# Kernel tuning notes

Hardware: AMD Instinct MI355X
Metric: run time of the kernel (lower is better)

## Reference

```python
import jax, jax.numpy as jnp
import numpy as np

B, N, C = 4, 2048, 1024
H = 16
D = C // H  # head_dim = 64
NEG = -1e9


def setup_inputs() -> dict:
    key = jax.random.key(0)
    k1, k2, k3, k4 = jax.random.split(key, 4)
    x = jax.random.normal(k1, (B, N, C), dtype=jnp.float32)
    # additive causal mask [N, N]: 0 on/below diagonal, -1e9 above
    causal = jnp.tril(jnp.ones((N, N), dtype=bool))
    attn_mask = jnp.where(causal, 0.0, NEG).astype(jnp.float32)
    # params: qkv Dense (no bias, qkv_bias=False), proj Dense (with bias)
    W_qkv = jax.random.normal(k2, (C, 3 * C), dtype=jnp.float32) / np.sqrt(C)
    W_proj = jax.random.normal(k3, (C, C), dtype=jnp.float32) / np.sqrt(C)
    b_proj = jnp.zeros((C,), dtype=jnp.float32)
    return {"x": x, "attn_mask": attn_mask, "W_qkv": W_qkv,
            "W_proj": W_proj, "b_proj": b_proj}


def reference(x, attn_mask, W_qkv, W_proj, b_proj):
    b, n, c = x.shape
    # qkv projection -> [B, N, 3, H, D] -> q,k,v each [B, H, N, D]
    qkv = (x @ W_qkv).reshape(b, n, 3, H, D)
    qkv = jnp.transpose(qkv, (2, 0, 3, 1, 4))
    q, k, v = qkv[0], qkv[1], qkv[2]
    # unfused attention: full [B, H, N, N] score matrix
    scores = jnp.einsum('bhnd,bhmd->bhnm', q, k) / np.sqrt(D).astype(jnp.float32)
    scores = scores + attn_mask  # broadcast [N, N] over batch/heads
    attn_w = jax.nn.softmax(scores.astype(jnp.float32), axis=-1).astype(scores.dtype)
    out = jnp.einsum('bhnm,bhmd->bhnd', attn_w, v)
    out = jnp.transpose(out, (0, 2, 1, 3)).reshape(b, n, c)
    return out @ W_proj + b_proj
```

## Files before the change

kernel.cpp:

```cpp
#include <hip/hip_runtime.h>
#include <stdint.h>


typedef short s16x8 __attribute__((ext_vector_type(8)));
typedef short s16x4 __attribute__((ext_vector_type(4)));
typedef float f32x4 __attribute__((ext_vector_type(4)));
typedef unsigned int u32;

__device__ __forceinline__ uint16_t f2bf(float f) {
  union { float f; uint32_t u; } v; v.f = f;
  uint32_t r = v.u + 0x7fffu + ((v.u >> 16) & 1u);
  return (uint16_t)(r >> 16);
}

__device__ __forceinline__ u32 cvt_pk_bf16(float lo, float hi) {
  u32 r;
  asm("v_cvt_pk_bf16_f32 %0, %1, %2" : "=v"(r) : "v"(lo), "v"(hi));
  return r;
}

__device__ __forceinline__ s16x8 pack4(u32 w0, u32 w1, u32 w2, u32 w3) {
  union { u32 u[4]; s16x8 v; } t;
  t.u[0] = w0; t.u[1] = w1; t.u[2] = w2; t.u[3] = w3;
  return t.v;
}

__device__ __forceinline__ s16x8 pack2h(s16x4 a, s16x4 b) {
  union { s16x4 h[2]; s16x8 v; } t;
  t.h[0] = a; t.h[1] = b;
  return t.v;
}

#define GLOAD_LDS16(g, l)                                            \
  __builtin_amdgcn_global_load_lds(                                  \
      (const __attribute__((address_space(1))) void*)(g),            \
      (__attribute__((address_space(3))) void*)(l), 16, 0, 0)

__device__ __forceinline__ void transpose32_body(
    const float* __restrict__ src, uint16_t* __restrict__ dst,
    int R, int C, int bx32, int by32, uint16_t (*tile)[33], int tid) {
  const int tx = tid & 31, ty = tid >> 5;
#pragma unroll
  for (int i = 0; i < 32; i += 8)
    tile[ty + i][tx] = f2bf(src[(size_t)(by32 + ty + i) * C + bx32 + tx]);
  __syncthreads();
#pragma unroll
  for (int i = 0; i < 32; i += 8)
    dst[(size_t)(bx32 + ty + i) * R + by32 + tx] = tile[tx][ty + i];
}

__global__ __launch_bounds__(256) void prep_kernel(
    const float* __restrict__ x, uint16_t* __restrict__ xbf,
    const float* __restrict__ Wqkv, uint16_t* __restrict__ wqkvT,
    const float* __restrict__ Wproj, uint16_t* __restrict__ wprojT) {
  __shared__ uint16_t tile[32][33];
  const int bid = blockIdx.x;
  if (bid < 4096) {
    const int i = bid * 256 + threadIdx.x;
    const f32x4 a = ((const f32x4*)x)[2 * i];
    const f32x4 b = ((const f32x4*)x)[2 * i + 1];
    s16x8 r;
    r[0] = (short)f2bf(a[0]); r[1] = (short)f2bf(a[1]);
    r[2] = (short)f2bf(a[2]); r[3] = (short)f2bf(a[3]);
    r[4] = (short)f2bf(b[0]); r[5] = (short)f2bf(b[1]);
    r[6] = (short)f2bf(b[2]); r[7] = (short)f2bf(b[3]);
    ((s16x8*)xbf)[i] = r;
  } else if (bid < 4096 + 3072) {
    const int t = bid - 4096;
    transpose32_body(Wqkv, wqkvT, 1024, 3072, (t % 96) * 32, (t / 96) * 32,
                     tile, threadIdx.x);
  } else {
    const int t = bid - 7168;
    transpose32_body(Wproj, wprojT, 1024, 1024, (t & 31) * 32, (t >> 5) * 32,
                     tile, threadIdx.x);
  }
}

__global__ __launch_bounds__(256) void vtrans_kernel(
    const uint16_t* __restrict__ src, uint16_t* __restrict__ dst) {
  const int bh = blockIdx.y >> 1, dhalf = blockIdx.y & 1;
  const int n0 = blockIdx.x * 32, d0 = dhalf * 32;
  const uint16_t* sb = src + (size_t)bh * 131072;
  uint16_t* db = dst + (size_t)bh * 131072;
  __shared__ uint16_t tile[32][33];
  const int tx = threadIdx.x & 31, ty = threadIdx.x >> 5;
#pragma unroll
  for (int i = 0; i < 32; i += 8)
    tile[ty + i][tx] = sb[(size_t)(n0 + ty + i) * 64 + d0 + tx];
  __syncthreads();
#pragma unroll
  for (int i = 0; i < 32; i += 8)
    db[(size_t)(d0 + ty + i) * 2048 + n0 + tx] = tile[tx][ty + i];
}

template <bool ROUTE>
__global__ __launch_bounds__(256) void gemm_bt_kernel(
    const uint16_t* __restrict__ A, const uint16_t* __restrict__ Bt,
    float* __restrict__ Cout,
    uint16_t* __restrict__ rq, uint16_t* __restrict__ rk, uint16_t* __restrict__ rv,
    const float* __restrict__ bias, int M, int N, int K) {
  __shared__ uint16_t sA[128 * 64];
  __shared__ uint16_t sB[128 * 64];
  const int tid = threadIdx.x;
  const int lane = tid & 63, w = tid >> 6;
  const int l15 = lane & 15, quad = lane >> 4;
  const int row0 = blockIdx.y * 128, col0 = blockIdx.x * 128;
  const int wm = (w >> 1) * 64, wn = (w & 1) * 64;

  f32x4 acc[4][4];
#pragma unroll
  for (int i = 0; i < 4; ++i)
#pragma unroll
    for (int j = 0; j < 4; ++j)
#pragma unroll
      for (int e = 0; e < 4; ++e) acc[i][j][e] = 0.0f;

  const int sx = l15 & 7;
  const int ok[2] = {((0 * 4 + quad) ^ sx) * 8, ((1 * 4 + quad) ^ sx) * 8};

  for (int k0 = 0; k0 < K; k0 += 64) {
    __syncthreads();
#pragma unroll
    for (int i = 0; i < 4; ++i) {
      const int cbase = i * 256 + w * 64;
      const int c = cbase + lane;
      const int r = c >> 3;
      const int kc = ((c & 7) ^ (r & 7)) * 8;
      GLOAD_LDS16(A + (size_t)(row0 + r) * K + k0 + kc, sA + cbase * 8);
      GLOAD_LDS16(Bt + (size_t)(col0 + r) * K + k0 + kc, sB + cbase * 8);
    }
    __syncthreads();

#pragma unroll
    for (int kk = 0; kk < 2; ++kk) {
      s16x8 aF[4], bF[4];
#pragma unroll
      for (int mt = 0; mt < 4; ++mt)
        aF[mt] = *(const s16x8*)(sA + (wm + mt * 16 + l15) * 64 + ok[kk]);
#pragma unroll
      for (int nt = 0; nt < 4; ++nt)
        bF[nt] = *(const s16x8*)(sB + (wn + nt * 16 + l15) * 64 + ok[kk]);
#pragma unroll
      for (int mt = 0; mt < 4; ++mt)
#pragma unroll
        for (int nt = 0; nt < 4; ++nt)
          acc[mt][nt] = __builtin_amdgcn_mfma_f32_16x16x32_bf16(aF[mt], bF[nt], acc[mt][nt], 0, 0, 0);
    }
  }

  if (ROUTE) {
    const int which = col0 >> 10;
    uint16_t* dst = (which == 0) ? rq : ((which == 1) ? rk : rv);
    const float qs = (which == 0) ? 0.18033688011112042f : 1.0f;
#pragma unroll
    for (int mt = 0; mt < 4; ++mt) {
#pragma unroll
      for (int nt = 0; nt < 4; ++nt) {
        const int colg0 = col0 + wn + nt * 16;
        const int h = (colg0 >> 6) & 15, d0 = colg0 & 63;
#pragma unroll
        for (int i = 0; i < 4; ++i) {
          const int rowg = row0 + wm + mt * 16 + quad * 4 + i;
          const int bh = ((rowg >> 11) << 4) + h, n = rowg & 2047;
          dst[(size_t)bh * 131072 + (size_t)n * 64 + d0 + l15] = f2bf(acc[mt][nt][i] * qs);
        }
      }
    }
  } else {
#pragma unroll
    for (int mt = 0; mt < 4; ++mt) {
#pragma unroll
      for (int nt = 0; nt < 4; ++nt) {
        const int colg = col0 + wn + nt * 16 + l15;
        const float bv = bias[colg];
#pragma unroll
        for (int i = 0; i < 4; ++i) {
          const int rowg = row0 + wm + mt * 16 + quad * 4 + i;
          Cout[(size_t)rowg * N + colg] = acc[mt][nt][i] + bv;
        }
      }
    }
  }
}

__global__ __launch_bounds__(256) void attn_kernel(
    const uint16_t* __restrict__ q_ws, const uint16_t* __restrict__ k_ws,
    const uint16_t* __restrict__ vt_ws, uint16_t* __restrict__ out) {
  const int p = blockIdx.x;
  const int bh = blockIdx.y;
  const int b = bh >> 4, h = bh & 15;
  const int q0L = p * 64, q0H = (31 - p) * 64;
  const int tid = threadIdx.x;
  const int lane = tid & 63, w = tid >> 6;
  const int l15 = lane & 15, quad = lane >> 4;

  const uint16_t* qb = q_ws + (size_t)bh * 131072;
  const uint16_t* kb = k_ws + (size_t)bh * 131072;
  const uint16_t* vtb = vt_ws + (size_t)bh * 131072;

  __shared__ uint16_t sK[2][64 * 72];
  __shared__ uint16_t sV[2][64 * 72];

  const int qrowL = q0L + w * 16 + l15;
  const int qrowH = q0H + w * 16 + l15;
  const s16x8 aQL0 = *(const s16x8*)(qb + (size_t)qrowL * 64 + quad * 8);
  const s16x8 aQL1 = *(const s16x8*)(qb + (size_t)qrowL * 64 + 32 + quad * 8);
  const s16x8 aQH0 = *(const s16x8*)(qb + (size_t)qrowH * 64 + quad * 8);
  const s16x8 aQH1 = *(const s16x8*)(qb + (size_t)qrowH * 64 + 32 + quad * 8);

  f32x4 oL[4], oH[4], laccL, laccH;
#pragma unroll
  for (int e = 0; e < 4; ++e) { laccL[e] = 0.0f; laccH[e] = 0.0f; }
#pragma unroll
  for (int i = 0; i < 4; ++i)
#pragma unroll
    for (int e = 0; e < 4; ++e) { oL[i][e] = 0.0f; oH[i][e] = 0.0f; }

  s16x8 bOnes;
#pragma unroll
  for (int j = 0; j < 8; ++j) bOnes[j] = (short)0x3F80;

  const int vr = tid >> 2, dc = (tid & 3) * 16;
  s16x8 rk0 = *(const s16x8*)(kb + (size_t)vr * 64 + dc);
  s16x8 rk1 = *(const s16x8*)(kb + (size_t)vr * 64 + dc + 8);
  s16x8 rv0 = *(const s16x8*)(vtb + (size_t)vr * 2048 + dc);
  s16x8 rv1 = *(const s16x8*)(vtb + (size_t)vr * 2048 + dc + 8);

  const int qrel = w * 16 + l15;

  auto qkt = [&](const s16x8& a0, const s16x8& a1, const uint16_t* sKb,
                 f32x4 (&s)[4]) {
#pragma unroll
    for (int nt = 0; nt < 4; ++nt) {
      f32x4 z;
#pragma unroll
      for (int e = 0; e < 4; ++e) z[e] = 0.0f;
      const s16x8 bK0 = *(const s16x8*)(sKb + (nt * 16 + l15) * 72 + quad * 8);
      const s16x8 bK1 = *(const s16x8*)(sKb + (nt * 16 + l15) * 72 + 32 + quad * 8);
      s[nt] = __builtin_amdgcn_mfma_f32_16x16x32_bf16(bK0, a0, z, 0, 0, 0);
      s[nt] = __builtin_amdgcn_mfma_f32_16x16x32_bf16(bK1, a1, s[nt], 0, 0, 0);
    }
  };

  auto finish = [&](const f32x4 (&s)[4], bool diag, f32x4* o, f32x4& lacc,
                    const uint16_t* sVb) {
#pragma unroll
    for (int kk = 0; kk < 2; ++kk) {
      u32 wlo[2], whi[2];
#pragma unroll
      for (int t2 = 0; t2 < 2; ++t2) {
        const f32x4& sv = s[2 * kk + t2];
        float pp[4];
        if (diag) {
          const int nt = 2 * kk + t2;
#pragma unroll
          for (int i = 0; i < 4; ++i) {
            const int kv = nt * 16 + quad * 4 + i;
            pp[i] = (kv > qrel) ? 0.0f : __builtin_amdgcn_exp2f(sv[i]);
          }
        } else {
#pragma unroll
          for (int i = 0; i < 4; ++i) pp[i] = __builtin_amdgcn_exp2f(sv[i]);
        }
        wlo[t2] = cvt_pk_bf16(pp[0], pp[1]);
        whi[t2] = cvt_pk_bf16(pp[2], pp[3]);
      }
      const s16x8 aP = pack4(wlo[0], whi[0], wlo[1], whi[1]);
      lacc = __builtin_amdgcn_mfma_f32_16x16x32_bf16(aP, bOnes, lacc, 0, 0, 0);
#pragma unroll
      for (int dblk = 0; dblk < 4; ++dblk) {
        const uint16_t* vrow = sVb + (dblk * 16 + l15) * 72 + kk * 32 + quad * 4;
        const s16x4 b0 = *(const s16x4*)(vrow);
        const s16x4 b1 = *(const s16x4*)(vrow + 16);
        const s16x8 bV = pack2h(b0, b1);
        o[dblk] = __builtin_amdgcn_mfma_f32_16x16x32_bf16(aP, bV, o[dblk], 0, 0, 0);
      }
    }
  };

  const int TH = q0H >> 6;
  const int TL = q0L >> 6;
  f32x4 sHp[4];

  for (int t = 0; t <= TH; ++t) {
    const int buf = t & 1;
    uint16_t* sKb = sK[buf];
    uint16_t* sVb = sV[buf];
    *(s16x8*)(sKb + vr * 72 + dc) = rk0;
    *(s16x8*)(sKb + vr * 72 + dc + 8) = rk1;
    *(s16x8*)(sVb + vr * 72 + dc) = rv0;
    *(s16x8*)(sVb + vr * 72 + dc + 8) = rv1;
    if (t < TH) {
      const int kvn = (t + 1) << 6;
      rk0 = *(const s16x8*)(kb + (size_t)(kvn + vr) * 64 + dc);
      rk1 = *(const s16x8*)(kb + (size_t)(kvn + vr) * 64 + dc + 8);
      rv0 = *(const s16x8*)(vtb + (size_t)vr * 2048 + kvn + dc);
      rv1 = *(const s16x8*)(vtb + (size_t)vr * 2048 + kvn + dc + 8);
    }
    if (t >= 1) finish(sHp, false, oH, laccH, sV[buf ^ 1]);
    __syncthreads();
    qkt(aQH0, aQH1, sKb, sHp);
    if (t <= TL) {
      f32x4 sLt[4];
      qkt(aQL0, aQL1, sKb, sLt);
      finish(sLt, t == TL, oL, laccL, sVb);
    }
  }
  finish(sHp, true, oH, laccH, sV[TH & 1]);

  const size_t obase = (size_t)b * 2048 * 1024 + (size_t)h * 64;
  auto epi = [&](f32x4* o, const f32x4& lacc, int q0) {
#pragma unroll
    for (int i = 0; i < 4; ++i) {
      const float invi = 1.0f / lacc[i];
      const int row = q0 + w * 16 + quad * 4 + i;
#pragma unroll
      for (int dblk = 0; dblk < 4; ++dblk)
        out[obase + (size_t)row * 1024 + dblk * 16 + l15] = f2bf(o[dblk][i] * invi);
    }
  };
  epi(oH, laccH, q0H);
  epi(oL, laccL, q0L);
}

extern "C" void kernel_launch(void* const* d_in, const int* in_sizes, int n_in,
                              void* d_out, int out_size, void* d_ws, size_t ws_size,
                              hipStream_t stream) {
  (void)in_sizes; (void)n_in; (void)out_size; (void)ws_size;
  const float* x     = (const float*)d_in[0];
  const float* Wqkv  = (const float*)d_in[2];
  const float* Wproj = (const float*)d_in[3];
  const float* bproj = (const float*)d_in[4];
  float* outp = (float*)d_out;

  uint16_t* ws      = (uint16_t*)d_ws;
  uint16_t* q_ws    = ws;
  uint16_t* k_ws    = ws + (size_t)8388608;
  uint16_t* v_ws    = ws + (size_t)16777216;
  uint16_t* attn_ws = ws + (size_t)16777216;
  uint16_t* wqkvT   = ws + (size_t)25165824;
  uint16_t* wprojT  = ws + (size_t)28311552;
  uint16_t* xbf     = (uint16_t*)d_out;
  uint16_t* vt_ws   = (uint16_t*)d_out;

  prep_kernel<<<8192, 256, 0, stream>>>(x, xbf, Wqkv, wqkvT, Wproj, wprojT);
  gemm_bt_kernel<true><<<dim3(24, 64), 256, 0, stream>>>(
      xbf, wqkvT, nullptr, q_ws, k_ws, v_ws, nullptr, 8192, 3072, 1024);
  vtrans_kernel<<<dim3(64, 128), 256, 0, stream>>>(v_ws, vt_ws);
  attn_kernel<<<dim3(16, 64), 256, 0, stream>>>(q_ws, k_ws, vt_ws, attn_ws);
  gemm_bt_kernel<false><<<dim3(8, 64), 256, 0, stream>>>(
      attn_ws, wprojT, outp, nullptr, nullptr, nullptr, bproj, 8192, 1024, 1024);
}
```

Before: 272.1 us.

## XOR-swizzle shared K/V tiles and software-pipeline low-tile softmax/PV

Replaces the padded 72-stride shared-memory layout for K and V^T with an unpadded 64-stride layout that uses an XOR swizzle on 8-element chunks. This avoids LDS bank conflicts and shrinks shared memory. It also defers the low query tile's exp/PV step by one iteration, matching the high tile, so its QK^T MFMAs can overlap with the previous tile's softmax and PV work. The cost is more live registers for the extra score array and more complex address arithmetic.

```diff
diff --git a/kernel.cpp b/kernel.cpp
--- a/kernel.cpp
+++ b/kernel.cpp
@@ -198,8 +198,8 @@
   const uint16_t* kb = k_ws + (size_t)bh * 131072;
   const uint16_t* vtb = vt_ws + (size_t)bh * 131072;
 
-  __shared__ uint16_t sK[2][64 * 72];
-  __shared__ uint16_t sV[2][64 * 72];
+  __shared__ uint16_t sK[2][64 * 64];
+  __shared__ uint16_t sV[2][64 * 64];
 
   const int qrowL = q0L + w * 16 + l15;
   const int qrowH = q0H + w * 16 + l15;
@@ -221,11 +221,21 @@
   for (int j = 0; j < 8; ++j) bOnes[j] = (short)0x3F80;
 
   const int vr = tid >> 2, dc = (tid & 3) * 16;
+  const int wc0 = ((tid & 3) * 2 + 0) ^ (vr & 7);
+  const int wc1 = ((tid & 3) * 2 + 1) ^ (vr & 7);
   s16x8 rk0 = *(const s16x8*)(kb + (size_t)vr * 64 + dc);
   s16x8 rk1 = *(const s16x8*)(kb + (size_t)vr * 64 + dc + 8);
   s16x8 rv0 = *(const s16x8*)(vtb + (size_t)vr * 2048 + dc);
   s16x8 rv1 = *(const s16x8*)(vtb + (size_t)vr * 2048 + dc + 8);
 
+  const int sx = l15 & 7;
+  const int okK0 = (quad ^ sx) * 8;
+  const int okK1 = ((quad + 4) ^ sx) * 8;
+  const int ovA[2] = {((0 + (quad >> 1)) ^ sx) * 8 + (quad & 1) * 4,
+                      ((4 + (quad >> 1)) ^ sx) * 8 + (quad & 1) * 4};
+  const int ovB[2] = {((2 + (quad >> 1)) ^ sx) * 8 + (quad & 1) * 4,
+                      ((6 + (quad >> 1)) ^ sx) * 8 + (quad & 1) * 4};
+
   const int qrel = w * 16 + l15;
 
   auto qkt = [&](const s16x8& a0, const s16x8& a1, const uint16_t* sKb,
@@ -235,8 +245,8 @@
       f32x4 z;
 #pragma unroll
       for (int e = 0; e < 4; ++e) z[e] = 0.0f;
-      const s16x8 bK0 = *(const s16x8*)(sKb + (nt * 16 + l15) * 72 + quad * 8);
-      const s16x8 bK1 = *(const s16x8*)(sKb + (nt * 16 + l15) * 72 + 32 + quad * 8);
+      const s16x8 bK0 = *(const s16x8*)(sKb + (nt * 16 + l15) * 64 + okK0);
+      const s16x8 bK1 = *(const s16x8*)(sKb + (nt * 16 + l15) * 64 + okK1);
       s[nt] = __builtin_amdgcn_mfma_f32_16x16x32_bf16(bK0, a0, z, 0, 0, 0);
       s[nt] = __builtin_amdgcn_mfma_f32_16x16x32_bf16(bK1, a1, s[nt], 0, 0, 0);
     }
@@ -269,9 +279,9 @@
       lacc = __builtin_amdgcn_mfma_f32_16x16x32_bf16(aP, bOnes, lacc, 0, 0, 0);
 #pragma unroll
       for (int dblk = 0; dblk < 4; ++dblk) {
-        const uint16_t* vrow = sVb + (dblk * 16 + l15) * 72 + kk * 32 + quad * 4;
-        const s16x4 b0 = *(const s16x4*)(vrow);
-        const s16x4 b1 = *(const s16x4*)(vrow + 16);
+        const uint16_t* vrow = sVb + (dblk * 16 + l15) * 64;
+        const s16x4 b0 = *(const s16x4*)(vrow + ovA[kk]);
+        const s16x4 b1 = *(const s16x4*)(vrow + ovB[kk]);
         const s16x8 bV = pack2h(b0, b1);
         o[dblk] = __builtin_amdgcn_mfma_f32_16x16x32_bf16(aP, bV, o[dblk], 0, 0, 0);
       }
@@ -280,16 +290,16 @@
 
   const int TH = q0H >> 6;
   const int TL = q0L >> 6;
-  f32x4 sHp[4];
+  f32x4 sHp[4], sLp[4];
 
   for (int t = 0; t <= TH; ++t) {
     const int buf = t & 1;
     uint16_t* sKb = sK[buf];
     uint16_t* sVb = sV[buf];
-    *(s16x8*)(sKb + vr * 72 + dc) = rk0;
-    *(s16x8*)(sKb + vr * 72 + dc + 8) = rk1;
-    *(s16x8*)(sVb + vr * 72 + dc) = rv0;
-    *(s16x8*)(sVb + vr * 72 + dc + 8) = rv1;
+    *(s16x8*)(sKb + vr * 64 + wc0 * 8) = rk0;
+    *(s16x8*)(sKb + vr * 64 + wc1 * 8) = rk1;
+    *(s16x8*)(sVb + vr * 64 + wc0 * 8) = rv0;
+    *(s16x8*)(sVb + vr * 64 + wc1 * 8) = rv1;
     if (t < TH) {
       const int kvn = (t + 1) << 6;
       rk0 = *(const s16x8*)(kb + (size_t)(kvn + vr) * 64 + dc);
@@ -297,14 +307,13 @@
       rv0 = *(const s16x8*)(vtb + (size_t)vr * 2048 + kvn + dc);
       rv1 = *(const s16x8*)(vtb + (size_t)vr * 2048 + kvn + dc + 8);
     }
-    if (t >= 1) finish(sHp, false, oH, laccH, sV[buf ^ 1]);
+    if (t >= 1) {
+      finish(sHp, false, oH, laccH, sV[buf ^ 1]);
+      if (t - 1 <= TL) finish(sLp, (t - 1) == TL, oL, laccL, sV[buf ^ 1]);
+    }
     __syncthreads();
     qkt(aQH0, aQH1, sKb, sHp);
-    if (t <= TL) {
-      f32x4 sLt[4];
-      qkt(aQL0, aQL1, sKb, sLt);
-      finish(sLt, t == TL, oL, laccL, sVb);
-    }
+    if (t <= TL) qkt(aQL0, aQL1, sKb, sLp);
   }
   finish(sHp, true, oH, laccH, sV[TH & 1]);
 
```

Result: no change. 271.4 us (-0.3%).
